# Performance work log

Hardware: AMD Instinct MI355X
Metric: run time of the kernel (lower is better)

Reference implementation:

```python
import jax, jax.numpy as jnp
import numpy as np
import math


def _local_band_mask(L):
    # window_size = ceil(1.2 * log2(L) / 2); True where attention is DISALLOWED
    w = math.ceil(1.2 * np.log2(L) / 2)
    i = jnp.arange(L)[:, None]
    j = jnp.arange(L)[None, :]
    return jnp.abs(i - j) > w  # [L, L] bool, True outside the band


def setup_inputs() -> dict:
    key = jax.random.key(0)
    kq, kk, kv = jax.random.split(key, 3)
    B, L, H, E = 2, 2048, 8, 64
    return {
        "queries": jax.random.normal(kq, (B, L, H, E), dtype=jnp.float32),
        "keys": jax.random.normal(kk, (B, L, H, E), dtype=jnp.float32),
        "values": jax.random.normal(kv, (B, L, H, E), dtype=jnp.float32),
    }


def reference(queries, keys, values):
    # queries/keys: [B, L, H, E], values: [B, L, H, D]
    B, L, H, E = queries.shape
    scale = 1.0 / math.sqrt(E)
    # scores: [B, H, L, L]
    scores = jnp.einsum("bqhe,bkhe->bhqk", queries, keys) * scale
    mask = _local_band_mask(L)  # [L, L]
    scores = jnp.where(mask[None, None, :, :], -jnp.inf, scores)
    attn = jax.nn.softmax(scores, axis=-1)  # dropout is identity in eval
    # output: [B, L, H, D]
    out = jnp.einsum("bhqk,bkhd->bqhd", attn, values)
    return out
```

## Files before the change

### kernel.cpp

```cpp
#include <hip/hip_runtime.h>
#include <math.h>


constexpr int L_DIM = 2048;
constexpr int H_DIM = 8;
constexpr int E_DIM = 64;
constexpr int W = 7;
constexpr int NK = 2 * W + 1;
constexpr int TQ = 64;
constexpr int HALO = 8;
constexpr int ROWS = TQ + 2 * HALO;

template <int CTRL>
__device__ __forceinline__ float dpp_add(float s) {
  int t = __builtin_amdgcn_mov_dpp(__builtin_bit_cast(int, s), CTRL, 0xF, 0xF, true);
  return s + __builtin_bit_cast(float, t);
}

__global__ __launch_bounds__(512, 4) void local_attn_kernel(
    const float* __restrict__ q,
    const float* __restrict__ k,
    const float* __restrict__ v,
    float* __restrict__ out) {
  __shared__ float ks[ROWS * E_DIM];

  const int cpx = gridDim.x >> 3;
  const int bid = (blockIdx.x & 7) * cpx + (blockIdx.x >> 3);

  const int tile = bid & (L_DIM / TQ - 1);
  const int bh = bid >> 5;
  const int h = bh & (H_DIM - 1);
  const int b = bh >> 3;
  const int l0 = tile * TQ;

  const int tid = threadIdx.x;
  const int wv = tid >> 6;
  const int lane = tid & 63;
  const int qsub = lane >> 3;
  const int c = lane & 7;

  const size_t bhb = (size_t)b * L_DIM * H_DIM + h;

  const int rsub = lane >> 4;
  const int c4 = lane & 15;
#pragma unroll
  for (int t = 0; t < 3; ++t) {
    const int ch = wv + t * 8;
    if (ch < 20) {
      const int rl = ch * 4 + rsub;
      int rg = l0 - HALO + rl;
      rg = rg < 0 ? 0 : (rg > L_DIM - 1 ? L_DIM - 1 : rg);
      const float4 val =
          *(const float4*)(k + ((bhb + (size_t)rg * H_DIM) << 6) + c4 * 4);
      *(float4*)&ks[(rl * 16 + (c4 ^ (rl & 7))) * 4] = val;
    }
  }

  const int l0w = l0 + wv * 8;
  const int l = l0w + qsub;
  const float* qp = q + ((bhb + (size_t)l * H_DIM) << 6) + c * 8;
  float4 q0 = *(const float4*)qp;
  float4 q1 = *(const float4*)(qp + 4);
  const float scale = 0.125f;
  q0.x *= scale; q0.y *= scale; q0.z *= scale; q0.w *= scale;
  q1.x *= scale; q1.y *= scale; q1.z *= scale; q1.w *= scale;

  __syncthreads();

  const int base_rl = wv * 8 + 1 + qsub;
  float sc[NK];
#pragma unroll
  for (int j = 0; j < NK; ++j) {
    const int rl = base_rl + j;
    const int s8 = rl & 7;
    const float4 k0 = *(const float4*)&ks[(rl * 16 + ((2 * c) ^ s8)) * 4];
    const float4 k1 = *(const float4*)&ks[(rl * 16 + ((2 * c + 1) ^ s8)) * 4];
    float s = q0.x * k0.x + q0.y * k0.y + q0.z * k0.z + q0.w * k0.w +
              q1.x * k1.x + q1.y * k1.y + q1.z * k1.z + q1.w * k1.w;
    s = dpp_add<0xB1>(s);
    s = dpp_add<0x4E>(s);
    s = dpp_add<0x141>(s);
    const int kk = l0w + qsub - W + j;
    sc[j] = ((unsigned)kk < (unsigned)L_DIM) ? s : -INFINITY;
  }

  float mx = sc[0];
#pragma unroll
  for (int j = 1; j < NK; ++j) mx = fmaxf(mx, sc[j]);
  float den = 0.0f;
#pragma unroll
  for (int j = 0; j < NK; ++j) {
    sc[j] = __expf(sc[j] - mx);
    den += sc[j];
  }
  const float inv = __builtin_amdgcn_rcpf(den);

  float4 a0 = {0.f, 0.f, 0.f, 0.f};
  float4 a1 = {0.f, 0.f, 0.f, 0.f};
#pragma unroll
  for (int j = 0; j < NK; ++j) {
    int kk = l0w + qsub - W + j;
    kk = kk < 0 ? 0 : (kk > L_DIM - 1 ? L_DIM - 1 : kk);
    const float* vp = v + ((bhb + (size_t)kk * H_DIM) << 6) + c * 8;
    const float4 v0 = *(const float4*)vp;
    const float4 v1 = *(const float4*)(vp + 4);
    const float p = sc[j];
    a0.x += p * v0.x; a0.y += p * v0.y; a0.z += p * v0.z; a0.w += p * v0.w;
    a1.x += p * v1.x; a1.y += p * v1.y; a1.z += p * v1.z; a1.w += p * v1.w;
  }

  float* op = out + ((bhb + (size_t)l * H_DIM) << 6) + c * 8;
  a0.x *= inv; a0.y *= inv; a0.z *= inv; a0.w *= inv;
  a1.x *= inv; a1.y *= inv; a1.z *= inv; a1.w *= inv;
  *(float4*)op = a0;
  *(float4*)(op + 4) = a1;
}

extern "C" void kernel_launch(void* const* d_in, const int* in_sizes, int n_in,
                              void* d_out, int out_size, void* d_ws, size_t ws_size,
                              hipStream_t stream) {
  const float* q = (const float*)d_in[0];
  const float* k = (const float*)d_in[1];
  const float* v = (const float*)d_in[2];
  float* out = (float*)d_out;

  const int B = in_sizes[0] / (L_DIM * H_DIM * E_DIM);
  const int blocks = B * H_DIM * (L_DIM / TQ);

  local_attn_kernel<<<blocks, 512, 0, stream>>>(q, k, v, out);
}
```

Baseline: 13.28 us.

## Stage V in shared memory, halve query tile, use 16 lanes per query

Halves the query tile to 32 rows per block, so there are twice as many blocks, and stages both the K and V halo rows in swizzled shared memory. The weighted V sum now reads from LDS instead of issuing 15 strided global loads per query. Each query is now handled by 16 lanes holding a float4 each instead of 8 lanes holding two float4s, which needs one extra DPP reduction step. The halo overhead per tile grows with the smaller tile, so more redundant K/V loading is traded for removing repeated global V reads and for higher occupancy.

```diff
diff --git a/kernel.cpp b/kernel.cpp
--- a/kernel.cpp
+++ b/kernel.cpp
@@ -7,9 +7,10 @@
 constexpr int E_DIM = 64;
 constexpr int W = 7;
 constexpr int NK = 2 * W + 1;
-constexpr int TQ = 64;
+constexpr int TQ = 32;
 constexpr int HALO = 8;
 constexpr int ROWS = TQ + 2 * HALO;
+constexpr int NCH = ROWS / 4;
 
 template <int CTRL>
 __device__ __forceinline__ float dpp_add(float s) {
@@ -17,18 +18,19 @@
   return s + __builtin_bit_cast(float, t);
 }
 
-__global__ __launch_bounds__(512, 4) void local_attn_kernel(
+__global__ __launch_bounds__(512, 8) void local_attn_kernel(
     const float* __restrict__ q,
     const float* __restrict__ k,
     const float* __restrict__ v,
     float* __restrict__ out) {
   __shared__ float ks[ROWS * E_DIM];
+  __shared__ float vs[ROWS * E_DIM];
 
   const int cpx = gridDim.x >> 3;
   const int bid = (blockIdx.x & 7) * cpx + (blockIdx.x >> 3);
 
   const int tile = bid & (L_DIM / TQ - 1);
-  const int bh = bid >> 5;
+  const int bh = bid >> 6;
   const int h = bh & (H_DIM - 1);
   const int b = bh >> 3;
   const int l0 = tile * TQ;
@@ -36,50 +38,44 @@
   const int tid = threadIdx.x;
   const int wv = tid >> 6;
   const int lane = tid & 63;
-  const int qsub = lane >> 3;
-  const int c = lane & 7;
+  const int qsub = lane >> 4;
+  const int c4 = lane & 15;
 
   const size_t bhb = (size_t)b * L_DIM * H_DIM + h;
 
   const int rsub = lane >> 4;
-  const int c4 = lane & 15;
 #pragma unroll
   for (int t = 0; t < 3; ++t) {
     const int ch = wv + t * 8;
-    if (ch < 20) {
-      const int rl = ch * 4 + rsub;
-      int rg = l0 - HALO + rl;
-      rg = rg < 0 ? 0 : (rg > L_DIM - 1 ? L_DIM - 1 : rg);
-      const float4 val =
-          *(const float4*)(k + ((bhb + (size_t)rg * H_DIM) << 6) + c4 * 4);
-      *(float4*)&ks[(rl * 16 + (c4 ^ (rl & 7))) * 4] = val;
-    }
+    const int m = (ch >= NCH) ? 1 : 0;
+    const int cc = ch - m * NCH;
+    const int rl = cc * 4 + rsub;
+    int rg = l0 - HALO + rl;
+    rg = rg < 0 ? 0 : (rg > L_DIM - 1 ? L_DIM - 1 : rg);
+    const float4 val =
+        *(const float4*)((m ? v : k) + ((bhb + (size_t)rg * H_DIM) << 6) + c4 * 4);
+    *(float4*)&((m ? vs : ks)[(rl * 16 + (c4 ^ (rl & 7))) * 4]) = val;
   }
 
-  const int l0w = l0 + wv * 8;
+  const int l0w = l0 + wv * 4;
   const int l = l0w + qsub;
-  const float* qp = q + ((bhb + (size_t)l * H_DIM) << 6) + c * 8;
-  float4 q0 = *(const float4*)qp;
-  float4 q1 = *(const float4*)(qp + 4);
+  float4 q0 = *(const float4*)(q + ((bhb + (size_t)l * H_DIM) << 6) + c4 * 4);
   const float scale = 0.125f;
   q0.x *= scale; q0.y *= scale; q0.z *= scale; q0.w *= scale;
-  q1.x *= scale; q1.y *= scale; q1.z *= scale; q1.w *= scale;
 
   __syncthreads();
 
-  const int base_rl = wv * 8 + 1 + qsub;
+  const int base_rl = wv * 4 + 1 + qsub;
   float sc[NK];
 #pragma unroll
   for (int j = 0; j < NK; ++j) {
     const int rl = base_rl + j;
-    const int s8 = rl & 7;
-    const float4 k0 = *(const float4*)&ks[(rl * 16 + ((2 * c) ^ s8)) * 4];
-    const float4 k1 = *(const float4*)&ks[(rl * 16 + ((2 * c + 1) ^ s8)) * 4];
-    float s = q0.x * k0.x + q0.y * k0.y + q0.z * k0.z + q0.w * k0.w +
-              q1.x * k1.x + q1.y * k1.y + q1.z * k1.z + q1.w * k1.w;
+    const float4 k0 = *(const float4*)&ks[(rl * 16 + (c4 ^ (rl & 7))) * 4];
+    float s = q0.x * k0.x + q0.y * k0.y + q0.z * k0.z + q0.w * k0.w;
     s = dpp_add<0xB1>(s);
     s = dpp_add<0x4E>(s);
     s = dpp_add<0x141>(s);
+    s = dpp_add<0x140>(s);
     const int kk = l0w + qsub - W + j;
     sc[j] = ((unsigned)kk < (unsigned)L_DIM) ? s : -INFINITY;
   }
@@ -96,24 +92,17 @@
   const float inv = __builtin_amdgcn_rcpf(den);
 
   float4 a0 = {0.f, 0.f, 0.f, 0.f};
-  float4 a1 = {0.f, 0.f, 0.f, 0.f};
 #pragma unroll
   for (int j = 0; j < NK; ++j) {
-    int kk = l0w + qsub - W + j;
-    kk = kk < 0 ? 0 : (kk > L_DIM - 1 ? L_DIM - 1 : kk);
-    const float* vp = v + ((bhb + (size_t)kk * H_DIM) << 6) + c * 8;
-    const float4 v0 = *(const float4*)vp;
-    const float4 v1 = *(const float4*)(vp + 4);
+    const int rl = base_rl + j;
+    const float4 v0 = *(const float4*)&vs[(rl * 16 + (c4 ^ (rl & 7))) * 4];
     const float p = sc[j];
     a0.x += p * v0.x; a0.y += p * v0.y; a0.z += p * v0.z; a0.w += p * v0.w;
-    a1.x += p * v1.x; a1.y += p * v1.y; a1.z += p * v1.z; a1.w += p * v1.w;
   }
 
-  float* op = out + ((bhb + (size_t)l * H_DIM) << 6) + c * 8;
+  float* op = out + ((bhb + (size_t)l * H_DIM) << 6) + c4 * 4;
   a0.x *= inv; a0.y *= inv; a0.z *= inv; a0.w *= inv;
-  a1.x *= inv; a1.y *= inv; a1.z *= inv; a1.w *= inv;
   *(float4*)op = a0;
-  *(float4*)(op + 4) = a1;
 }
 
 extern "C" void kernel_launch(void* const* d_in, const int* in_sizes, int n_in,
```

Result: faster. 12.20 us (-8.1%).
